# Kernel tuning notes

Measured on AMD Instinct MI355X. Metric: run time of the kernel, lower is better.

The kernel has to match this reference:

```python
import jax, jax.numpy as jnp
import numpy as np

B, K, D = 128, 64, 1536        # batch, image regions, CNN feature dim
EM, H, A = 512, 1024, 1024     # embedding, hidden, attention dims
VOCAB, MAX_LEN = 10000, 30


def setup_inputs() -> dict:
    key = jax.random.key(0)
    ks = jax.random.split(key, 20)
    def p(i, shape):
        return jax.random.normal(ks[i], shape, dtype=jnp.float32) * 0.02
    z = lambda *s: jnp.zeros(s, jnp.float32)
    return {
        "im_input": jax.random.normal(ks[0], (B, K, D), dtype=jnp.float32),
        "w_input": jax.random.randint(ks[1], (B, MAX_LEN + 1), 0, VOCAB),
        "caption_lengths": jax.random.randint(ks[2], (B,), 2, MAX_LEN + 2),
        "emb": p(3, (VOCAB, EM)),
        "W_enc": p(4, (D, H)), "b_enc": z(H),
        "W_glob": p(5, (D, EM)), "b_glob": z(EM),
        "W_ih": p(6, (2 * EM, 4 * H)), "b_ih": z(4 * H),
        "W_hh": p(7, (H, 4 * H)), "b_hh": z(4 * H),
        "W_xg": p(8, (2 * EM, H)), "b_xg": z(H),
        "W_hg": p(9, (H, H)), "b_hg": z(H),
        "Wv": p(10, (H, A)), "bv": z(A),
        "Ws": p(11, (H, A)), "bs": z(A),
        "Wh": p(12, (H, A)), "bh": z(A),
        "wa": p(13, (A, 1)), "ba": z(1),
        "W_out": p(14, (H, VOCAB)), "b_out": z(VOCAB),
    }


def _forward(im_input, emb, W_enc, b_enc, W_glob, b_glob, W_ih, b_ih, W_hh, b_hh,
             W_xg, b_xg, W_hg, b_hg, Wv, bv, Ws, bs, Wh, bh, wa, ba, W_out, b_out,
             w_input, caption_lengths):
    # ImageEncoder: per-region features (B,K,H) and global feature (B,EM)
    V = jax.nn.relu(jnp.einsum('bkd,dh->bkh', im_input, W_enc) + b_enc)
    g = jax.nn.relu(jnp.mean(im_input, axis=1) @ W_glob + b_glob)
    # sort batch by caption length, descending (as in the torch forward)
    order = jnp.argsort(-caption_lengths)
    w = w_input[order]
    g = g[order]
    V = V[order]
    lens = caption_lengths[order] - 1  # has_end_seq_token=True
    target = w[:, 1:]
    h0 = jnp.zeros((B, H), jnp.float32)
    c0 = jnp.zeros((B, H), jnp.float32)

    # Full-batch scan is math-equivalent to the dynamic batch_size_t slicing:
    # lengths are sorted descending, so rows that go inactive never become
    # active again; their masked predictions stay zero, matching the original.
    def step(carry, t):
        h, c = carry
        x = jnp.concatenate([emb[w[:, t]], g], axis=1)  # (B, 2*EM)
        # SentinelLSTM: standard LSTM cell + visual sentinel gate
        gates = x @ W_ih + b_ih + h @ W_hh + b_hh
        i_g, f_g, g_g, o_g = jnp.split(gates, 4, axis=1)
        c_new = jax.nn.sigmoid(f_g) * c + jax.nn.sigmoid(i_g) * jnp.tanh(g_g)
        h_new = jax.nn.sigmoid(o_g) * jnp.tanh(c_new)
        s = jax.nn.sigmoid(x @ W_xg + b_xg + h @ W_hg + b_hg) * jnp.tanh(c_new)
        # Adaptive attention over K regions + sentinel
        hp = h_new @ Wh + bh                                      # (B,A)
        zv = (jnp.tanh(V @ Wv + bv + hp[:, None, :]) @ wa)[..., 0] + ba  # (B,K)
        zs = jnp.tanh(s @ Ws + bs + hp) @ wa + ba                  # (B,1)
        alpha = jax.nn.softmax(jnp.concatenate([zv, zs], axis=1), axis=1)  # (B,K+1)
        ctx = jnp.einsum('bk,bkh->bh', alpha[:, :-1], V)
        beta = alpha[:, -1:]
        z_t = beta * s + (1.0 - beta) * ctx + h_new
        # MultimodalDecoder (decoding_stack_size=1 -> single projection)
        probs = jax.nn.softmax(z_t @ W_out + b_out, axis=1)        # (B,VOCAB)
        probs = jnp.where((t < lens)[:, None], probs, 0.0)
        return (h_new, c_new), probs

    _, P = jax.lax.scan(step, (h0, c0), jnp.arange(MAX_LEN))
    predictions = jnp.transpose(P, (1, 0, 2))  # (B, MAX_LEN, VOCAB)
    return predictions, target, lens


def reference(im_input, w_input, caption_lengths, emb, W_enc, b_enc, W_glob, b_glob,
              W_ih, b_ih, W_hh, b_hh, W_xg, b_xg, W_hg, b_hg, Wv, bv, Ws, bs,
              Wh, bh, wa, ba, W_out, b_out):
    return _forward(im_input, emb, W_enc, b_enc, W_glob, b_glob, W_ih, b_ih,
                    W_hh, b_hh, W_xg, b_xg, W_hg, b_hg, Wv, bv, Ws, bs, Wh, bh,
                    wa, ba, W_out, b_out, w_input, caption_lengths)
```

## Files before the change

### kernel.cpp

```cpp
#include <hip/hip_runtime.h>
#include <math.h>

#define NB 128
#define NKK 64
#define ND 1536
#define NEM 512
#define NH 1024
#define NVOC 10000
#define NT 30
#define CHT 6

#define BM 128
#define BN 64
#define BK 64

typedef __bf16 bf16x8 __attribute__((ext_vector_type(8)));
typedef __bf16 bf16x4 __attribute__((ext_vector_type(4)));
typedef float f32x4 __attribute__((ext_vector_type(4)));

__device__ __forceinline__ float ftanh(float x) {
    float e = __expf(2.f * x);
    return 1.f - 2.f * __builtin_amdgcn_rcpf(e + 1.f);
}
__device__ __forceinline__ float fsig(float x) {
    return __builtin_amdgcn_rcpf(1.f + __expf(-x));
}

__global__ void sort_kernel(const int* __restrict__ cap, const int* __restrict__ w,
                            float* __restrict__ out_target, float* __restrict__ out_lens,
                            int* __restrict__ order, int* __restrict__ lens_s,
                            int* __restrict__ widx) {
    __shared__ int lcap[NB];
    __shared__ int sord[NB];
    int b = threadIdx.x;
    lcap[b] = cap[b];
    __syncthreads();
    int lb = lcap[b];
    int pos = 0;
    for (int j = 0; j < NB; j++) {
        int lj = lcap[j];
        if (lj > lb || (lj == lb && j < b)) pos++;
    }
    sord[pos] = b;
    __syncthreads();
    int src = sord[b];
    order[b] = src;
    int ln = lcap[src] - 1;
    lens_s[b] = ln;
    out_lens[b] = (float)ln;
    for (int j = 0; j < NT; j++)
        out_target[b * NT + j] = (float)w[src * (NT + 1) + j + 1];
    for (int t = 0; t < NT; t++)
        widx[t * NB + b] = w[src * (NT + 1) + t];
}

__global__ void init_kernel(float* __restrict__ c, float* __restrict__ ghh0,
                            float* __restrict__ ghh1) {
    int tid = blockIdx.x * 256 + threadIdx.x;
    if (tid < NB * NH) c[tid] = 0.f;
    if (tid < NB * 5120) { ghh0[tid] = 0.f; ghh1[tid] = 0.f; }
}

__global__ void meanim_kernel(const float* __restrict__ im, const int* __restrict__ order,
                              __bf16* __restrict__ meanb) {
    int b = blockIdx.x;
    int src = order[b];
    const float* base = im + (size_t)src * NKK * ND;
    for (int d = threadIdx.x; d < ND; d += 256) {
        float acc = 0.f;
        for (int k = 0; k < NKK; k++) acc += base[(size_t)k * ND + d];
        meanb[b * ND + d] = (__bf16)(acc * (1.0f / NKK));
    }
}

__global__ void conv_perm_kernel(const float* __restrict__ im, const int* __restrict__ order,
                                 __bf16* __restrict__ imb) {
    int e8 = blockIdx.x * 256 + threadIdx.x;
    size_t elem = (size_t)e8 * 8;
    int bp = (int)(elem / (NKK * ND));
    size_t rem = elem % (NKK * ND);
    const float* src = im + (size_t)order[bp] * NKK * ND + rem;
    float4 f0 = *(const float4*)(src);
    float4 f1 = *(const float4*)(src + 4);
    bf16x8 v = {(__bf16)f0.x, (__bf16)f0.y, (__bf16)f0.z, (__bf16)f0.w,
                (__bf16)f1.x, (__bf16)f1.y, (__bf16)f1.z, (__bf16)f1.w};
    *(bf16x8*)(imb + elem) = v;
}

__global__ __launch_bounds__(256) void transpose_pack(
    const float* __restrict__ src, int ldn, int K, int N,
    __bf16* __restrict__ dst, int ldk) {
    __shared__ float tile[64][65];
    int k0 = blockIdx.y * 64, n0 = blockIdx.x * 64;
    int t = threadIdx.x;
    int kr = t >> 2, nc0 = (t & 3) * 16;
    int kk = k0 + kr;
#pragma unroll
    for (int j = 0; j < 16; j += 4) {
        int nn = n0 + nc0 + j;
        float4 v = make_float4(0.f, 0.f, 0.f, 0.f);
        if (kk < K && nn + 3 < N) v = *(const float4*)(src + (size_t)kk * ldn + nn);
        else if (kk < K) {
            float tmp[4] = {0.f, 0.f, 0.f, 0.f};
            for (int q = 0; q < 4; q++) if (nn + q < N) tmp[q] = src[(size_t)kk * ldn + nn + q];
            v = make_float4(tmp[0], tmp[1], tmp[2], tmp[3]);
        }
        tile[kr][nc0 + j + 0] = v.x; tile[kr][nc0 + j + 1] = v.y;
        tile[kr][nc0 + j + 2] = v.z; tile[kr][nc0 + j + 3] = v.w;
    }
    __syncthreads();
    int nr = t >> 2, kc0 = (t & 3) * 16;
    if (n0 + nr < N) {
        __bf16* drow = dst + (size_t)(n0 + nr) * ldk + k0 + kc0;
#pragma unroll
        for (int j = 0; j < 16; j++)
            if (k0 + kc0 + j < K) drow[j] = (__bf16)tile[kc0 + j][nr];
    }
}

__global__ void conv_bf16_vec(const float* __restrict__ src, __bf16* __restrict__ dst, int n4) {
    int id = blockIdx.x * 256 + threadIdx.x;
    if (id < n4) {
        float4 v = *(const float4*)(src + (size_t)id * 4);
        __bf16* d = dst + (size_t)id * 4;
        d[0] = (__bf16)v.x; d[1] = (__bf16)v.y; d[2] = (__bf16)v.z; d[3] = (__bf16)v.w;
    }
}

__global__ void pack_biases(const float* __restrict__ b_ih, const float* __restrict__ b_hh,
                            const float* __restrict__ b_xg, const float* __restrict__ b_hg,
                            const float* __restrict__ bh, const float* __restrict__ bs,
                            float* __restrict__ bstep, float* __restrict__ b2) {
    int i = blockIdx.x * 256 + threadIdx.x;
    if (i < 4096) bstep[i] = b_ih[i] + b_hh[i];
    else bstep[i] = b_xg[i - 4096] + b_hg[i - 4096];
    if (i < 1024) b2[i] = bh[i];
    else if (i < 2048) b2[i] = bs[i - 1024];
}

template <int AMODE, bool RELU, bool OUTBF>
__global__ __launch_bounds__(256) void gemm_k(
    const void* __restrict__ Aptr, int lda,
    const __bf16* __restrict__ Bt, int ldb,
    const float* __restrict__ bias,
    void* __restrict__ Cptr, int ldc,
    int N, int K,
    const int* __restrict__ widx,
    const __bf16* __restrict__ embb, const __bf16* __restrict__ gbf,
    int swz) {
    const int t = threadIdx.x;
    const int lane = t & 63;
    const int wid = t >> 6;
    const int wr = wid >> 1, wc = wid & 1;
    int bx = blockIdx.x, by = blockIdx.y;
    if (swz) {
        int L = by * gridDim.x + bx;
        int xcd = L & 7, q = L >> 3;
        by = xcd * (gridDim.y >> 3) + q / gridDim.x;
        bx = q % gridDim.x;
    }
    const int m0 = by * BM;
    const int n0 = bx * BN;
    const int lr = lane & 15, lg = lane >> 4, lr8 = lr & 7;

    __shared__ __bf16 As[BM * BK];
    __shared__ __bf16 Bs[BN * BK];

    f32x4 acc[4][2];
#pragma unroll
    for (int i = 0; i < 4; i++)
#pragma unroll
        for (int j = 0; j < 2; j++) acc[i][j] = (f32x4){0.f, 0.f, 0.f, 0.f};

    const int s_row = t >> 1;
    const int s_g0 = (t & 1) * 4;
    const int s_col = t >> 2;
    const int s_bg0 = (t & 3) * 2;
    const int r8 = s_row & 7, c8 = s_col & 7;
    const int aw0 = (s_row << 6) + (((s_g0 + 0) ^ r8) << 3);
    const int aw1 = (s_row << 6) + (((s_g0 + 1) ^ r8) << 3);
    const int aw2 = (s_row << 6) + (((s_g0 + 2) ^ r8) << 3);
    const int aw3 = (s_row << 6) + (((s_g0 + 3) ^ r8) << 3);
    const int bw0 = (s_col << 6) + (((s_bg0 + 0) ^ c8) << 3);
    const int bw1 = (s_col << 6) + (((s_bg0 + 1) ^ c8) << 3);
    const int rA0 = (wr * 64 + 0 * 16 + lr) << 6;
    const int rA1 = (wr * 64 + 1 * 16 + lr) << 6;
    const int rA2 = (wr * 64 + 2 * 16 + lr) << 6;
    const int rA3 = (wr * 64 + 3 * 16 + lr) << 6;
    const int cB0 = (wc * 32 + 0 * 16 + lr) << 6;
    const int cB1 = (wc * 32 + 1 * 16 + lr) << 6;

    const __bf16* a_srcb = nullptr;
    const __bf16* e_base = nullptr;
    const __bf16* g_base = nullptr;
    if (AMODE == 1) {
        int r = m0 + s_row;
        e_base = embb + (size_t)widx[r] * NEM + s_g0 * 8;
        g_base = gbf + (size_t)(r & 127) * NEM + s_g0 * 8 - NEM;
    } else {
        a_srcb = (const __bf16*)Aptr + (size_t)(m0 + s_row) * lda + s_g0 * 8;
    }
    const __bf16* b_src = Bt + (size_t)(n0 + s_col) * ldb + s_bg0 * 8;
    const bool b_ok = (n0 + s_col) < N;

    auto loadA = [&](int k0, bf16x8& a0, bf16x8& a1, bf16x8& a2, bf16x8& a3) {
        if (AMODE == 1) {
            int kk = k0 + s_g0 * 8;
            const bf16x8* p = (const bf16x8*)((kk < NEM ? e_base : g_base) + k0);
            a0 = p[0]; a1 = p[1]; a2 = p[2]; a3 = p[3];
        } else {
            const bf16x8* p = (const bf16x8*)(a_srcb + k0);
            a0 = p[0]; a1 = p[1]; a2 = p[2]; a3 = p[3];
        }
    };
    auto loadB = [&](int k0, bf16x8& b0, bf16x8& b1) {
        if (b_ok) {
            const bf16x8* p = (const bf16x8*)(b_src + k0);
            b0 = p[0]; b1 = p[1];
        } else {
            bf16x8 zv = {};
            b0 = zv; b1 = zv;
        }
    };
    auto writeS = [&](bf16x8 a0, bf16x8 a1, bf16x8 a2, bf16x8 a3, bf16x8 b0, bf16x8 b1) {
        *(bf16x8*)&As[aw0] = a0; *(bf16x8*)&As[aw1] = a1;
        *(bf16x8*)&As[aw2] = a2; *(bf16x8*)&As[aw3] = a3;
        *(bf16x8*)&Bs[bw0] = b0; *(bf16x8*)&Bs[bw1] = b1;
    };
    auto compute = [&]() {
#pragma unroll
        for (int ks = 0; ks < 2; ks++) {
            const int gsw = ((ks * 4 + lg) ^ lr8) << 3;
            bf16x8 af0 = *(const bf16x8*)&As[rA0 + gsw];
            bf16x8 af1 = *(const bf16x8*)&As[rA1 + gsw];
            bf16x8 af2 = *(const bf16x8*)&As[rA2 + gsw];
            bf16x8 af3 = *(const bf16x8*)&As[rA3 + gsw];
            bf16x8 bv0 = *(const bf16x8*)&Bs[cB0 + gsw];
            bf16x8 bv1 = *(const bf16x8*)&Bs[cB1 + gsw];
            acc[0][0] = __builtin_amdgcn_mfma_f32_16x16x32_bf16(af0, bv0, acc[0][0], 0, 0, 0);
            acc[0][1] = __builtin_amdgcn_mfma_f32_16x16x32_bf16(af0, bv1, acc[0][1], 0, 0, 0);
            acc[1][0] = __builtin_amdgcn_mfma_f32_16x16x32_bf16(af1, bv0, acc[1][0], 0, 0, 0);
            acc[1][1] = __builtin_amdgcn_mfma_f32_16x16x32_bf16(af1, bv1, acc[1][1], 0, 0, 0);
            acc[2][0] = __builtin_amdgcn_mfma_f32_16x16x32_bf16(af2, bv0, acc[2][0], 0, 0, 0);
            acc[2][1] = __builtin_amdgcn_mfma_f32_16x16x32_bf16(af2, bv1, acc[2][1], 0, 0, 0);
            acc[3][0] = __builtin_amdgcn_mfma_f32_16x16x32_bf16(af3, bv0, acc[3][0], 0, 0, 0);
            acc[3][1] = __builtin_amdgcn_mfma_f32_16x16x32_bf16(af3, bv1, acc[3][1], 0, 0, 0);
        }
    };

    bf16x8 a0, a1, a2, a3, b0, b1;
    bf16x8 c0, c1, c2, c3, d0, d1;
    loadA(0, a0, a1, a2, a3);
    loadB(0, b0, b1);
    for (int k0 = 0; k0 < K; k0 += 2 * BK) {
        writeS(a0, a1, a2, a3, b0, b1);
        __syncthreads();
        loadA(k0 + BK, c0, c1, c2, c3);
        loadB(k0 + BK, d0, d1);
        compute();
        __syncthreads();
        writeS(c0, c1, c2, c3, d0, d1);
        __syncthreads();
        if (k0 + 2 * BK < K) {
            loadA(k0 + 2 * BK, a0, a1, a2, a3);
            loadB(k0 + 2 * BK, b0, b1);
        }
        compute();
        __syncthreads();
    }

    float* Cf = (float*)Cptr;
    __bf16* Cb = (__bf16*)Cptr;
#pragma unroll
    for (int mi = 0; mi < 4; mi++) {
#pragma unroll
        for (int ni = 0; ni < 2; ni++) {
            int col = n0 + wc * 32 + ni * 16 + lr;
            if (col < N) {
                float bb = bias[col];
#pragma unroll
                for (int rr = 0; rr < 4; rr++) {
                    int row = m0 + wr * 64 + mi * 16 + lg * 4 + rr;
                    float v = acc[mi][ni][rr] + bb;
                    if (RELU) v = fmaxf(v, 0.f);
                    if (OUTBF) Cb[(size_t)row * ldc + col] = (__bf16)v;
                    else Cf[(size_t)row * ldc + col] = v;
                }
            }
        }
    }
}

__device__ __forceinline__ void step_gemm(
    __bf16* As, __bf16* Bs,
    const __bf16* __restrict__ Ab, int lda,
    const __bf16* __restrict__ Bt, int ldb,
    const float* __restrict__ bias,
    float* __restrict__ C, int ldc, int N, int n0, int K) {
    const int t = threadIdx.x;
    const int lane = t & 63;
    const int wid = t >> 6;
    const int wr = wid >> 1, wc = wid & 1;
    const int lr = lane & 15, lg = lane >> 4, lr8 = lr & 7;

    f32x4 acc[4][2];
#pragma unroll
    for (int i = 0; i < 4; i++)
#pragma unroll
        for (int j = 0; j < 2; j++) acc[i][j] = (f32x4){0.f, 0.f, 0.f, 0.f};

    const int s_row = t >> 1;
    const int s_g0 = (t & 1) * 4;
    const int s_col = t >> 2;
    const int s_bg0 = (t & 3) * 2;
    const int r8 = s_row & 7, c8 = s_col & 7;
    const int aw0 = (s_row << 6) + (((s_g0 + 0) ^ r8) << 3);
    const int aw1 = (s_row << 6) + (((s_g0 + 1) ^ r8) << 3);
    const int aw2 = (s_row << 6) + (((s_g0 + 2) ^ r8) << 3);
    const int aw3 = (s_row << 6) + (((s_g0 + 3) ^ r8) << 3);
    const int bw0 = (s_col << 6) + (((s_bg0 + 0) ^ c8) << 3);
    const int bw1 = (s_col << 6) + (((s_bg0 + 1) ^ c8) << 3);
    const int rA0 = (wr * 64 + 0 * 16 + lr) << 6;
    const int rA1 = (wr * 64 + 1 * 16 + lr) << 6;
    const int rA2 = (wr * 64 + 2 * 16 + lr) << 6;
    const int rA3 = (wr * 64 + 3 * 16 + lr) << 6;
    const int cB0 = (wc * 32 + 0 * 16 + lr) << 6;
    const int cB1 = (wc * 32 + 1 * 16 + lr) << 6;

    const __bf16* a_src = Ab + (size_t)s_row * lda + s_g0 * 8;
    const __bf16* b_src = Bt + (size_t)(n0 + s_col) * ldb + s_bg0 * 8;
    const bool b_ok = (n0 + s_col) < N;

    auto loadA = [&](int k0, bf16x8& a0, bf16x8& a1, bf16x8& a2, bf16x8& a3) {
        const bf16x8* p = (const bf16x8*)(a_src + k0);
        a0 = p[0]; a1 = p[1]; a2 = p[2]; a3 = p[3];
    };
    auto loadB = [&](int k0, bf16x8& b0, bf16x8& b1) {
        if (b_ok) {
            const bf16x8* p = (const bf16x8*)(b_src + k0);
            b0 = p[0]; b1 = p[1];
        } else {
            bf16x8 zv = {};
            b0 = zv; b1 = zv;
        }
    };
    auto writeS = [&](bf16x8 a0, bf16x8 a1, bf16x8 a2, bf16x8 a3, bf16x8 b0, bf16x8 b1) {
        *(bf16x8*)&As[aw0] = a0; *(bf16x8*)&As[aw1] = a1;
        *(bf16x8*)&As[aw2] = a2; *(bf16x8*)&As[aw3] = a3;
        *(bf16x8*)&Bs[bw0] = b0; *(bf16x8*)&Bs[bw1] = b1;
    };
    auto compute = [&]() {
#pragma unroll
        for (int ks = 0; ks < 2; ks++) {
            const int gsw = ((ks * 4 + lg) ^ lr8) << 3;
            bf16x8 af0 = *(const bf16x8*)&As[rA0 + gsw];
            bf16x8 af1 = *(const bf16x8*)&As[rA1 + gsw];
            bf16x8 af2 = *(const bf16x8*)&As[rA2 + gsw];
            bf16x8 af3 = *(const bf16x8*)&As[rA3 + gsw];
            bf16x8 bv0 = *(const bf16x8*)&Bs[cB0 + gsw];
            bf16x8 bv1 = *(const bf16x8*)&Bs[cB1 + gsw];
            acc[0][0] = __builtin_amdgcn_mfma_f32_16x16x32_bf16(af0, bv0, acc[0][0], 0, 0, 0);
            acc[0][1] = __builtin_amdgcn_mfma_f32_16x16x32_bf16(af0, bv1, acc[0][1], 0, 0, 0);
            acc[1][0] = __builtin_amdgcn_mfma_f32_16x16x32_bf16(af1, bv0, acc[1][0], 0, 0, 0);
            acc[1][1] = __builtin_amdgcn_mfma_f32_16x16x32_bf16(af1, bv1, acc[1][1], 0, 0, 0);
            acc[2][0] = __builtin_amdgcn_mfma_f32_16x16x32_bf16(af2, bv0, acc[2][0], 0, 0, 0);
            acc[2][1] = __builtin_amdgcn_mfma_f32_16x16x32_bf16(af2, bv1, acc[2][1], 0, 0, 0);
            acc[3][0] = __builtin_amdgcn_mfma_f32_16x16x32_bf16(af3, bv0, acc[3][0], 0, 0, 0);
            acc[3][1] = __builtin_amdgcn_mfma_f32_16x16x32_bf16(af3, bv1, acc[3][1], 0, 0, 0);
        }
    };

    bf16x8 a0, a1, a2, a3, b0, b1;
    bf16x8 c0, c1, c2, c3, d0, d1;
    loadA(0, a0, a1, a2, a3);
    loadB(0, b0, b1);
    for (int k0 = 0; k0 < K; k0 += 2 * BK) {
        writeS(a0, a1, a2, a3, b0, b1);
        __syncthreads();
        loadA(k0 + BK, c0, c1, c2, c3);
        loadB(k0 + BK, d0, d1);
        compute();
        __syncthreads();
        writeS(c0, c1, c2, c3, d0, d1);
        __syncthreads();
        if (k0 + 2 * BK < K) {
            loadA(k0 + 2 * BK, a0, a1, a2, a3);
            loadB(k0 + 2 * BK, b0, b1);
        }
        compute();
        __syncthreads();
    }

#pragma unroll
    for (int mi = 0; mi < 4; mi++) {
#pragma unroll
        for (int ni = 0; ni < 2; ni++) {
            int col = n0 + wc * 32 + ni * 16 + lr;
            if (col < N) {
                float bb = bias ? bias[col] : 0.f;
#pragma unroll
                for (int rr = 0; rr < 4; rr++) {
                    int row = wr * 64 + mi * 16 + lg * 4 + rr;
                    C[(size_t)row * ldc + col] = acc[mi][ni][rr] + bb;
                }
            }
        }
    }
}

__global__ __launch_bounds__(256) void lstm_kernel(
    const __bf16* __restrict__ Xpre, const float* __restrict__ g0,
    const float* __restrict__ g1, float* __restrict__ c,
    __bf16* __restrict__ H_all, __bf16* __restrict__ S_all, int t) {
    int i4 = (blockIdx.x * 256 + threadIdx.x) * 4;
    int b = i4 >> 10, j = i4 & 1023;
    const __bf16* xp = Xpre + ((size_t)t * NB + b) * 5120 + j;
    const float* p0 = g0 + (size_t)b * 5120 + j;
    const float* p1 = g1 + (size_t)b * 5120 + j;
    bf16x4 xi = *(const bf16x4*)(xp);
    bf16x4 xf = *(const bf16x4*)(xp + 1024);
    bf16x4 xg = *(const bf16x4*)(xp + 2048);
    bf16x4 xo = *(const bf16x4*)(xp + 3072);
    bf16x4 xs = *(const bf16x4*)(xp + 4096);
    float4 gi0 = *(const float4*)(p0), gi1 = *(const float4*)(p1);
    float4 gf0 = *(const float4*)(p0 + 1024), gf1 = *(const float4*)(p1 + 1024);
    float4 gg0 = *(const float4*)(p0 + 2048), gg1 = *(const float4*)(p1 + 2048);
    float4 go0 = *(const float4*)(p0 + 3072), go1 = *(const float4*)(p1 + 3072);
    float4 gs0 = *(const float4*)(p0 + 4096), gs1 = *(const float4*)(p1 + 4096);
    float4 cv = *(const float4*)(c + i4);
    float ia[4] = {gi0.x + gi1.x, gi0.y + gi1.y, gi0.z + gi1.z, gi0.w + gi1.w};
    float fa[4] = {gf0.x + gf1.x, gf0.y + gf1.y, gf0.z + gf1.z, gf0.w + gf1.w};
    float ga[4] = {gg0.x + gg1.x, gg0.y + gg1.y, gg0.z + gg1.z, gg0.w + gg1.w};
    float oa[4] = {go0.x + go1.x, go0.y + go1.y, go0.z + go1.z, go0.w + go1.w};
    float sa[4] = {gs0.x + gs1.x, gs0.y + gs1.y, gs0.z + gs1.z, gs0.w + gs1.w};
    float cvp[4] = {cv.x, cv.y, cv.z, cv.w};
    float cn4[4];
    bf16x4 hv, sv;
#pragma unroll
    for (int e = 0; e < 4; e++) {
        float ig = fsig((float)xi[e] + ia[e]);
        float fg = fsig((float)xf[e] + fa[e]);
        float gv = ftanh((float)xg[e] + ga[e]);
        float og = fsig((float)xo[e] + oa[e]);
        float sg = fsig((float)xs[e] + sa[e]);
        float cn = fg * cvp[e] + ig * gv;
        float tc = ftanh(cn);
        cn4[e] = cn;
        hv[e] = (__bf16)(og * tc);
        sv[e] = (__bf16)(sg * tc);
    }
    *(float4*)(c + i4) = make_float4(cn4[0], cn4[1], cn4[2], cn4[3]);
    *(bf16x4*)(H_all + (size_t)t * NB * NH + i4) = hv;
    *(bf16x4*)(S_all + (size_t)t * NB * NH + i4) = sv;
}

__global__ __launch_bounds__(256) void gatesHH_kernel(
    const __bf16* __restrict__ H_t, const __bf16* __restrict__ Whh,
    float* __restrict__ g0, float* __restrict__ g1) {
    __shared__ __bf16 As[BM * BK];
    __shared__ __bf16 Bs[BN * BK];
    int kc = blockIdx.x & 1, n = blockIdx.x >> 1;
    step_gemm(As, Bs, H_t + kc * 512, NH, Whh + kc * 512, 2048, nullptr,
              kc == 0 ? g0 : g1, 5120, 5120, n * 64, 512);
}

__global__ __launch_bounds__(256) void attn_all_kernel(
    const __bf16* __restrict__ VA, const __bf16* __restrict__ V,
    const __bf16* __restrict__ HPa, const __bf16* __restrict__ SWSa,
    const float* __restrict__ wa, const __bf16* __restrict__ H_all,
    const __bf16* __restrict__ S_all, __bf16* __restrict__ Z_all) {
    __shared__ float zscore[NKK + 1];
    __shared__ float alpha_s[NKK + 1];
    int tb = blockIdx.x;
    int b = tb & 127;
    int wave = threadIdx.x >> 6, lane = threadIdx.x & 63;

    float hp_reg[16], wa_reg[16];
    {
        const bf16x8* hr = (const bf16x8*)(HPa + (size_t)tb * NH + lane * 16);
        bf16x8 h0 = hr[0], h1 = hr[1];
        const float* wb = wa + lane * 16;
#pragma unroll
        for (int q = 0; q < 4; q++) {
            float4 wv = *(const float4*)(wb + q * 4);
            wa_reg[q * 4 + 0] = wv.x; wa_reg[q * 4 + 1] = wv.y;
            wa_reg[q * 4 + 2] = wv.z; wa_reg[q * 4 + 3] = wv.w;
        }
#pragma unroll
        for (int j = 0; j < 8; j++) { hp_reg[j] = (float)h0[j]; hp_reg[8 + j] = (float)h1[j]; }
    }
    for (int k = wave; k <= NKK; k += 4) {
        float p = 0.f;
        if (k < NKK) {
            const bf16x8* row = (const bf16x8*)(VA + ((size_t)(b * NKK + k)) * NH + lane * 16);
            bf16x8 v0 = row[0], v1 = row[1];
#pragma unroll
            for (int j = 0; j < 8; j++) {
                p += ftanh((float)v0[j] + hp_reg[j]) * wa_reg[j];
                p += ftanh((float)v1[j] + hp_reg[8 + j]) * wa_reg[8 + j];
            }
        } else {
            const bf16x8* sr = (const bf16x8*)(SWSa + (size_t)tb * NH + lane * 16);
            bf16x8 s0 = sr[0], s1 = sr[1];
#pragma unroll
            for (int j = 0; j < 8; j++) {
                p += ftanh((float)s0[j] + hp_reg[j]) * wa_reg[j];
                p += ftanh((float)s1[j] + hp_reg[8 + j]) * wa_reg[8 + j];
            }
        }
        for (int off = 32; off; off >>= 1) p += __shfl_down(p, off);
        if (lane == 0) zscore[k] = p;
    }
    __syncthreads();
    if (threadIdx.x == 0) {
        float mx = zscore[0];
        for (int i = 1; i <= NKK; i++) mx = fmaxf(mx, zscore[i]);
        float ssum = 0.f;
        for (int i = 0; i <= NKK; i++) { float e = __expf(zscore[i] - mx); alpha_s[i] = e; ssum += e; }
        float inv = __builtin_amdgcn_rcpf(ssum);
        for (int i = 0; i <= NKK; i++) alpha_s[i] *= inv;
    }
    __syncthreads();
    float beta = alpha_s[NKK];
    {
        int jj0 = threadIdx.x * 4;
        const __bf16* vp = V + ((size_t)b * NKK) * NH + jj0;
        float c0 = 0.f, c1 = 0.f, c2 = 0.f, c3 = 0.f;
#pragma unroll 8
        for (int k = 0; k < NKK; k++) {
            bf16x4 vv = *(const bf16x4*)(vp + (size_t)k * NH);
            float a = alpha_s[k];
            c0 += a * (float)vv[0]; c1 += a * (float)vv[1];
            c2 += a * (float)vv[2]; c3 += a * (float)vv[3];
        }
        bf16x4 s4 = *(const bf16x4*)(S_all + (size_t)tb * NH + jj0);
        bf16x4 h4 = *(const bf16x4*)(H_all + (size_t)tb * NH + jj0);
        float ob = 1.f - beta;
        bf16x4 zv;
        zv[0] = (__bf16)(beta * (float)s4[0] + ob * c0 + (float)h4[0]);
        zv[1] = (__bf16)(beta * (float)s4[1] + ob * c1 + (float)h4[1]);
        zv[2] = (__bf16)(beta * (float)s4[2] + ob * c2 + (float)h4[2]);
        zv[3] = (__bf16)(beta * (float)s4[3] + ob * c3 + (float)h4[3]);
        *(bf16x4*)(Z_all + (size_t)tb * NH + jj0) = zv;
    }
}

__global__ __launch_bounds__(256) void softmax_chunk_kernel(
    const float* __restrict__ logitsC, const int* __restrict__ lens,
    float* __restrict__ pred, int t0) {
    __shared__ float se[NVOC];
    __shared__ float sred[4], sred2[4];
    int r = blockIdx.x;
    int tt = r >> 7, b = r & 127;
    int t = t0 + tt;
    float* out = pred + (size_t)b * NT * NVOC + (size_t)t * NVOC;
    if (t >= lens[b]) {
        for (int v = threadIdx.x; v < NVOC; v += 256) out[v] = 0.f;
        return;
    }
    const float* lg = logitsC + (size_t)r * NVOC;
    float mx = -1e30f;
    for (int v = threadIdx.x; v < NVOC; v += 256) {
        float x = lg[v];
        se[v] = x;
        mx = fmaxf(mx, x);
    }
    for (int off = 32; off; off >>= 1) mx = fmaxf(mx, __shfl_down(mx, off));
    if ((threadIdx.x & 63) == 0) sred[threadIdx.x >> 6] = mx;
    __syncthreads();
    mx = fmaxf(fmaxf(sred[0], sred[1]), fmaxf(sred[2], sred[3]));
    float ssum = 0.f;
    for (int v = threadIdx.x; v < NVOC; v += 256) {
        float e = __expf(se[v] - mx);
        se[v] = e;
        ssum += e;
    }
    for (int off = 32; off; off >>= 1) ssum += __shfl_down(ssum, off);
    if ((threadIdx.x & 63) == 0) sred2[threadIdx.x >> 6] = ssum;
    __syncthreads();
    ssum = sred2[0] + sred2[1] + sred2[2] + sred2[3];
    float inv = 1.f / ssum;
    for (int v = threadIdx.x; v < NVOC; v += 256) out[v] = se[v] * inv;
}

extern "C" void kernel_launch(void* const* d_in, const int* in_sizes, int n_in,
                              void* d_out, int out_size, void* d_ws, size_t ws_size,
                              hipStream_t stream) {
    const float* im = (const float*)d_in[0];
    const int* w_in = (const int*)d_in[1];
    const int* cap = (const int*)d_in[2];
    const float* emb = (const float*)d_in[3];
    const float* W_enc = (const float*)d_in[4];
    const float* b_enc = (const float*)d_in[5];
    const float* W_glob = (const float*)d_in[6];
    const float* b_glob = (const float*)d_in[7];
    const float* W_ih = (const float*)d_in[8];
    const float* b_ih = (const float*)d_in[9];
    const float* W_hh = (const float*)d_in[10];
    const float* b_hh = (const float*)d_in[11];
    const float* W_xg = (const float*)d_in[12];
    const float* b_xg = (const float*)d_in[13];
    const float* W_hg = (const float*)d_in[14];
    const float* b_hg = (const float*)d_in[15];
    const float* Wv = (const float*)d_in[16];
    const float* bv = (const float*)d_in[17];
    const float* Ws = (const float*)d_in[18];
    const float* bs = (const float*)d_in[19];
    const float* Wh = (const float*)d_in[20];
    const float* bh = (const float*)d_in[21];
    const float* wa = (const float*)d_in[22];
    const float* W_out = (const float*)d_in[24];
    const float* b_out = (const float*)d_in[25];

    float* out = (float*)d_out;
    float* pred = out;
    float* out_target = out + (size_t)NB * NT * NVOC;
    float* out_lens = out_target + NB * NT;

    char* p = (char*)d_ws;
    size_t off = 0;
    auto carve = [&](size_t bytes) {
        void* r = p + off;
        off += (bytes + 255) & ~(size_t)255;
        return r;
    };
    int* order = (int*)carve(NB * 4);
    int* lens_s = (int*)carve(NB * 4);
    int* widx = (int*)carve(NT * NB * 4);
    __bf16* embb = (__bf16*)carve((size_t)NVOC * NEM * 2);
    __bf16* Wstep_t = (__bf16*)carve((size_t)5120 * 2048 * 2);
    __bf16* W2t = (__bf16*)carve((size_t)2 * 1024 * 1024 * 2);
    __bf16* Wout_t = (__bf16*)carve((size_t)NVOC * 1024 * 2);
    __bf16* Wglob_t = (__bf16*)carve((size_t)512 * 1536 * 2);
    __bf16* Wenc_t = (__bf16*)carve((size_t)1024 * 1536 * 2);
    __bf16* Wv_t = (__bf16*)carve((size_t)1024 * 1024 * 2);
    float* bstep = (float*)carve(5120 * 4);
    float* b2 = (float*)carve(2048 * 4);
    __bf16* meanb = (__bf16*)carve((size_t)NB * ND * 2);
    __bf16* g_bf = (__bf16*)carve((size_t)NB * NEM * 2);
    __bf16* V_bf = (__bf16*)carve((size_t)NB * NKK * NH * 2);
    __bf16* VA_bf = (__bf16*)carve((size_t)NB * NKK * NH * 2);
    void* uni = carve((size_t)NT * NB * 5120 * 2);
    __bf16* imb = (__bf16*)uni;
    __bf16* Xpre = (__bf16*)uni;
    float* logitsC = (float*)uni;
    float* ghh0 = (float*)carve((size_t)NB * 5120 * 4);
    float* ghh1 = (float*)carve((size_t)NB * 5120 * 4);
    float* c = (float*)carve((size_t)NB * NH * 4);
    __bf16* H_all = (__bf16*)carve((size_t)NT * NB * NH * 2);
    __bf16* S_all = (__bf16*)carve((size_t)NT * NB * NH * 2);
    __bf16* HPa = (__bf16*)carve((size_t)NT * NB * NH * 2);
    __bf16* SWSa = (__bf16*)carve((size_t)NT * NB * NH * 2);
    __bf16* Z_all = (__bf16*)carve((size_t)NT * NB * NH * 2);
    if (off > ws_size) return;
    size_t off_save = off;
    float* logitsF = (float*)carve((size_t)NT * NB * NVOC * 4);
    bool useFull = (off <= ws_size);
    if (!useFull) off = off_save;

    sort_kernel<<<1, NB, 0, stream>>>(cap, w_in, out_target, out_lens, order, lens_s, widx);
    init_kernel<<<(NB * 5120 + 255) / 256, 256, 0, stream>>>(c, ghh0, ghh1);
    pack_biases<<<20, 256, 0, stream>>>(b_ih, b_hh, b_xg, b_hg, bh, bs, bstep, b2);
    conv_bf16_vec<<<(NVOC * NEM / 4 + 255) / 256, 256, 0, stream>>>(emb, embb, NVOC * NEM / 4);
    transpose_pack<<<dim3(8, 24), 256, 0, stream>>>(W_glob, 512, 1536, 512, Wglob_t, 1536);
    transpose_pack<<<dim3(16, 24), 256, 0, stream>>>(W_enc, 1024, 1536, 1024, Wenc_t, 1536);
    transpose_pack<<<dim3(16, 16), 256, 0, stream>>>(Wv, 1024, 1024, 1024, Wv_t, 1024);
    transpose_pack<<<dim3(64, 16), 256, 0, stream>>>(W_ih, 4096, 1024, 4096, Wstep_t, 2048);
    transpose_pack<<<dim3(64, 16), 256, 0, stream>>>(W_hh, 4096, 1024, 4096, Wstep_t + 1024, 2048);
    transpose_pack<<<dim3(16, 16), 256, 0, stream>>>(W_xg, 1024, 1024, 1024,
                                                     Wstep_t + (size_t)4096 * 2048, 2048);
    transpose_pack<<<dim3(16, 16), 256, 0, stream>>>(W_hg, 1024, 1024, 1024,
                                                     Wstep_t + (size_t)4096 * 2048 + 1024, 2048);
    transpose_pack<<<dim3(16, 16), 256, 0, stream>>>(Wh, 1024, 1024, 1024, W2t, 1024);
    transpose_pack<<<dim3(16, 16), 256, 0, stream>>>(Ws, 1024, 1024, 1024,
                                                     W2t + (size_t)1024 * 1024, 1024);
    transpose_pack<<<dim3(157, 16), 256, 0, stream>>>(W_out, NVOC, 1024, NVOC, Wout_t, 1024);
    meanim_kernel<<<NB, 256, 0, stream>>>(im, order, meanb);
    conv_perm_kernel<<<(NB * NKK * ND / 8) / 256, 256, 0, stream>>>(im, order, imb);

    gemm_k<0, true, true><<<dim3(NEM / BN, 1), 256, 0, stream>>>(
        meanb, ND, Wglob_t, ND, b_glob, g_bf, NEM, NEM, ND, nullptr, nullptr, nullptr, 0);
    gemm_k<0, true, true><<<dim3(NH / BN, (NB * NKK) / BM), 256, 0, stream>>>(
        imb, ND, Wenc_t, ND, b_enc, V_bf, NH, NH, ND, nullptr, nullptr, nullptr, 1);
    gemm_k<0, false, true><<<dim3(NH / BN, (NB * NKK) / BM), 256, 0, stream>>>(
        V_bf, NH, Wv_t, NH, bv, VA_bf, NH, NH, NH, nullptr, nullptr, nullptr, 1);
    gemm_k<1, false, true><<<dim3(5120 / BN, (NT * NB) / BM), 256, 0, stream>>>(
        nullptr, 0, Wstep_t, 2048, bstep, Xpre, 5120, 5120, 1024, widx, embb, g_bf, 0);

    for (int t = 0; t < NT; t++) {
        lstm_kernel<<<128, 256, 0, stream>>>(Xpre, ghh0, ghh1, c, H_all, S_all, t);
        if (t < NT - 1)
            gatesHH_kernel<<<160, 256, 0, stream>>>(
                H_all + (size_t)t * NB * NH, Wstep_t + 1024, ghh0, ghh1);
    }

    gemm_k<0, false, true><<<dim3(NH / BN, NT), 256, 0, stream>>>(
        H_all, NH, W2t, NH, b2, HPa, NH, NH, NH, nullptr, nullptr, nullptr, 0);
    gemm_k<0, false, true><<<dim3(NH / BN, NT), 256, 0, stream>>>(
        S_all, NH, W2t + (size_t)1024 * 1024, NH, b2 + 1024, SWSa, NH, NH, NH,
        nullptr, nullptr, nullptr, 0);
    attn_all_kernel<<<NT * NB, 256, 0, stream>>>(VA_bf, V_bf, HPa, SWSa, wa, H_all, S_all, Z_all);

    if (useFull) {
        gemm_k<0, false, false><<<dim3((NVOC + BN - 1) / BN, NT), 256, 0, stream>>>(
            Z_all, NH, Wout_t, NH, b_out, logitsF, NVOC, NVOC, NH, nullptr, nullptr, nullptr, 0);
        softmax_chunk_kernel<<<NT * NB, 256, 0, stream>>>(logitsF, lens_s, pred, 0);
    } else {
        for (int c5 = 0; c5 < NT / CHT; c5++) {
            gemm_k<0, false, false><<<dim3((NVOC + BN - 1) / BN, CHT), 256, 0, stream>>>(
                Z_all + (size_t)c5 * CHT * NB * NH, NH, Wout_t, NH, b_out, logitsC, NVOC,
                NVOC, NH, nullptr, nullptr, nullptr, 0);
            softmax_chunk_kernel<<<CHT * NB, 256, 0, stream>>>(logitsC, lens_s, pred, c5 * CHT);
        }
    }
}
```

Baseline: 1.069 ms.

## Fuse recurrent hidden GEMM with LSTM cell and batch attention projections

Each time step's split-K gatesHH GEMM and its separate elementwise LSTM kernel are replaced by one fused_step kernel. Each of its 16 blocks computes all five gate slices for 64 hidden units over the full K and then applies the cell update directly from registers. This removes the fp32 partial-gate buffers, their zero-init, and half of the per-step launches, but leaves only 16 workgroups busy during the serial recurrence. Separately, the two attention projection GEMMs are merged into one launch using blockIdx.z strides. A new XCD-aware block swizzle is used for the input-gate and output-vocabulary GEMMs, with the vocabulary grid padded to 160 columns.

```diff
diff --git a/kernel.cpp b/kernel.cpp
--- a/kernel.cpp
+++ b/kernel.cpp
@@ -54,11 +54,9 @@
         widx[t * NB + b] = w[src * (NT + 1) + t];
 }
 
-__global__ void init_kernel(float* __restrict__ c, float* __restrict__ ghh0,
-                            float* __restrict__ ghh1) {
+__global__ void init_kernel(float* __restrict__ c) {
     int tid = blockIdx.x * 256 + threadIdx.x;
     if (tid < NB * NH) c[tid] = 0.f;
-    if (tid < NB * 5120) { ghh0[tid] = 0.f; ghh1[tid] = 0.f; }
 }
 
 __global__ void meanim_kernel(const float* __restrict__ im, const int* __restrict__ order,
@@ -147,18 +145,25 @@
     int N, int K,
     const int* __restrict__ widx,
     const __bf16* __restrict__ embb, const __bf16* __restrict__ gbf,
-    int swz) {
+    int swz, size_t sA, size_t sB, size_t sBias, size_t sC) {
     const int t = threadIdx.x;
     const int lane = t & 63;
     const int wid = t >> 6;
     const int wr = wid >> 1, wc = wid & 1;
     int bx = blockIdx.x, by = blockIdx.y;
-    if (swz) {
+    if (swz == 1) {
         int L = by * gridDim.x + bx;
         int xcd = L & 7, q = L >> 3;
         by = xcd * (gridDim.y >> 3) + q / gridDim.x;
         bx = q % gridDim.x;
-    }
+    } else if (swz == 2) {
+        int L = by * gridDim.x + bx;
+        int xcd = L & 7, idx = L >> 3;
+        int nby = gridDim.y;
+        bx = xcd + 8 * (idx / nby);
+        by = idx % nby;
+    }
+    const int z = blockIdx.z;
     const int m0 = by * BM;
     const int n0 = bx * BN;
     const int lr = lane & 15, lg = lane >> 4, lr8 = lr & 7;
@@ -198,9 +203,9 @@
         e_base = embb + (size_t)widx[r] * NEM + s_g0 * 8;
         g_base = gbf + (size_t)(r & 127) * NEM + s_g0 * 8 - NEM;
     } else {
-        a_srcb = (const __bf16*)Aptr + (size_t)(m0 + s_row) * lda + s_g0 * 8;
-    }
-    const __bf16* b_src = Bt + (size_t)(n0 + s_col) * ldb + s_bg0 * 8;
+        a_srcb = (const __bf16*)Aptr + z * sA + (size_t)(m0 + s_row) * lda + s_g0 * 8;
+    }
+    const __bf16* b_src = Bt + z * sB + (size_t)(n0 + s_col) * ldb + s_bg0 * 8;
     const bool b_ok = (n0 + s_col) < N;
 
     auto loadA = [&](int k0, bf16x8& a0, bf16x8& a1, bf16x8& a2, bf16x8& a3) {
@@ -269,15 +274,16 @@
         __syncthreads();
     }
 
-    float* Cf = (float*)Cptr;
-    __bf16* Cb = (__bf16*)Cptr;
+    const float* bias_z = bias + z * sBias;
+    float* Cf = (float*)Cptr + z * sC;
+    __bf16* Cb = (__bf16*)Cptr + z * sC;
 #pragma unroll
     for (int mi = 0; mi < 4; mi++) {
 #pragma unroll
         for (int ni = 0; ni < 2; ni++) {
             int col = n0 + wc * 32 + ni * 16 + lr;
             if (col < N) {
-                float bb = bias[col];
+                float bb = bias_z[col];
 #pragma unroll
                 for (int rr = 0; rr < 4; rr++) {
                     int row = m0 + wr * 64 + mi * 16 + lg * 4 + rr;
@@ -291,177 +297,137 @@
     }
 }
 
-__device__ __forceinline__ void step_gemm(
-    __bf16* As, __bf16* Bs,
-    const __bf16* __restrict__ Ab, int lda,
-    const __bf16* __restrict__ Bt, int ldb,
-    const float* __restrict__ bias,
-    float* __restrict__ C, int ldc, int N, int n0, int K) {
-    const int t = threadIdx.x;
-    const int lane = t & 63;
-    const int wid = t >> 6;
+__global__ __launch_bounds__(256, 1) void fused_step(
+    const __bf16* __restrict__ Xpre, const __bf16* __restrict__ Hprev,
+    const __bf16* __restrict__ Wt,
+    float* __restrict__ c, __bf16* __restrict__ Hout, __bf16* __restrict__ Sout,
+    int t) {
+    const int tid = threadIdx.x;
+    const int lane = tid & 63;
+    const int wid = tid >> 6;
     const int wr = wid >> 1, wc = wid & 1;
     const int lr = lane & 15, lg = lane >> 4, lr8 = lr & 7;
-
-    f32x4 acc[4][2];
-#pragma unroll
-    for (int i = 0; i < 4; i++)
-#pragma unroll
-        for (int j = 0; j < 2; j++) acc[i][j] = (f32x4){0.f, 0.f, 0.f, 0.f};
-
-    const int s_row = t >> 1;
-    const int s_g0 = (t & 1) * 4;
-    const int s_col = t >> 2;
-    const int s_bg0 = (t & 3) * 2;
-    const int r8 = s_row & 7, c8 = s_col & 7;
-    const int aw0 = (s_row << 6) + (((s_g0 + 0) ^ r8) << 3);
-    const int aw1 = (s_row << 6) + (((s_g0 + 1) ^ r8) << 3);
-    const int aw2 = (s_row << 6) + (((s_g0 + 2) ^ r8) << 3);
-    const int aw3 = (s_row << 6) + (((s_g0 + 3) ^ r8) << 3);
-    const int bw0 = (s_col << 6) + (((s_bg0 + 0) ^ c8) << 3);
-    const int bw1 = (s_col << 6) + (((s_bg0 + 1) ^ c8) << 3);
-    const int rA0 = (wr * 64 + 0 * 16 + lr) << 6;
-    const int rA1 = (wr * 64 + 1 * 16 + lr) << 6;
-    const int rA2 = (wr * 64 + 2 * 16 + lr) << 6;
-    const int rA3 = (wr * 64 + 3 * 16 + lr) << 6;
-    const int cB0 = (wc * 32 + 0 * 16 + lr) << 6;
-    const int cB1 = (wc * 32 + 1 * 16 + lr) << 6;
-
-    const __bf16* a_src = Ab + (size_t)s_row * lda + s_g0 * 8;
-    const __bf16* b_src = Bt + (size_t)(n0 + s_col) * ldb + s_bg0 * 8;
-    const bool b_ok = (n0 + s_col) < N;
-
-    auto loadA = [&](int k0, bf16x8& a0, bf16x8& a1, bf16x8& a2, bf16x8& a3) {
-        const bf16x8* p = (const bf16x8*)(a_src + k0);
-        a0 = p[0]; a1 = p[1]; a2 = p[2]; a3 = p[3];
-    };
-    auto loadB = [&](int k0, bf16x8& b0, bf16x8& b1) {
-        if (b_ok) {
-            const bf16x8* p = (const bf16x8*)(b_src + k0);
-            b0 = p[0]; b1 = p[1];
-        } else {
-            bf16x8 zv = {};
-            b0 = zv; b1 = zv;
-        }
-    };
-    auto writeS = [&](bf16x8 a0, bf16x8 a1, bf16x8 a2, bf16x8 a3, bf16x8 b0, bf16x8 b1) {
-        *(bf16x8*)&As[aw0] = a0; *(bf16x8*)&As[aw1] = a1;
-        *(bf16x8*)&As[aw2] = a2; *(bf16x8*)&As[aw3] = a3;
-        *(bf16x8*)&Bs[bw0] = b0; *(bf16x8*)&Bs[bw1] = b1;
-    };
-    auto compute = [&]() {
-#pragma unroll
-        for (int ks = 0; ks < 2; ks++) {
-            const int gsw = ((ks * 4 + lg) ^ lr8) << 3;
-            bf16x8 af0 = *(const bf16x8*)&As[rA0 + gsw];
-            bf16x8 af1 = *(const bf16x8*)&As[rA1 + gsw];
-            bf16x8 af2 = *(const bf16x8*)&As[rA2 + gsw];
-            bf16x8 af3 = *(const bf16x8*)&As[rA3 + gsw];
-            bf16x8 bv0 = *(const bf16x8*)&Bs[cB0 + gsw];
-            bf16x8 bv1 = *(const bf16x8*)&Bs[cB1 + gsw];
-            acc[0][0] = __builtin_amdgcn_mfma_f32_16x16x32_bf16(af0, bv0, acc[0][0], 0, 0, 0);
-            acc[0][1] = __builtin_amdgcn_mfma_f32_16x16x32_bf16(af0, bv1, acc[0][1], 0, 0, 0);
-            acc[1][0] = __builtin_amdgcn_mfma_f32_16x16x32_bf16(af1, bv0, acc[1][0], 0, 0, 0);
-            acc[1][1] = __builtin_amdgcn_mfma_f32_16x16x32_bf16(af1, bv1, acc[1][1], 0, 0, 0);
-            acc[2][0] = __builtin_amdgcn_mfma_f32_16x16x32_bf16(af2, bv0, acc[2][0], 0, 0, 0);
-            acc[2][1] = __builtin_amdgcn_mfma_f32_16x16x32_bf16(af2, bv1, acc[2][1], 0, 0, 0);
-            acc[3][0] = __builtin_amdgcn_mfma_f32_16x16x32_bf16(af3, bv0, acc[3][0], 0, 0, 0);
-            acc[3][1] = __builtin_amdgcn_mfma_f32_16x16x32_bf16(af3, bv1, acc[3][1], 0, 0, 0);
-        }
-    };
-
-    bf16x8 a0, a1, a2, a3, b0, b1;
-    bf16x8 c0, c1, c2, c3, d0, d1;
-    loadA(0, a0, a1, a2, a3);
-    loadB(0, b0, b1);
-    for (int k0 = 0; k0 < K; k0 += 2 * BK) {
-        writeS(a0, a1, a2, a3, b0, b1);
-        __syncthreads();
-        loadA(k0 + BK, c0, c1, c2, c3);
-        loadB(k0 + BK, d0, d1);
-        compute();
-        __syncthreads();
-        writeS(c0, c1, c2, c3, d0, d1);
-        __syncthreads();
-        if (k0 + 2 * BK < K) {
-            loadA(k0 + 2 * BK, a0, a1, a2, a3);
-            loadB(k0 + 2 * BK, b0, b1);
-        }
-        compute();
-        __syncthreads();
-    }
-
-#pragma unroll
-    for (int mi = 0; mi < 4; mi++) {
-#pragma unroll
-        for (int ni = 0; ni < 2; ni++) {
-            int col = n0 + wc * 32 + ni * 16 + lr;
-            if (col < N) {
-                float bb = bias ? bias[col] : 0.f;
-#pragma unroll
-                for (int rr = 0; rr < 4; rr++) {
-                    int row = wr * 64 + mi * 16 + lg * 4 + rr;
-                    C[(size_t)row * ldc + col] = acc[mi][ni][rr] + bb;
+    const int j0 = blockIdx.x * 64;
+
+    __shared__ __bf16 As[BM * BK];
+    __shared__ __bf16 Bs[5 * BN * BK];
+
+    f32x4 acc[5][4][2];
+#pragma unroll
+    for (int q = 0; q < 5; q++)
+#pragma unroll
+        for (int i = 0; i < 4; i++)
+#pragma unroll
+            for (int j = 0; j < 2; j++) acc[q][i][j] = (f32x4){0.f, 0.f, 0.f, 0.f};
+
+    if (t > 0) {
+        const int s_row = tid >> 1;
+        const int s_g0 = (tid & 1) * 4;
+        const int s_col = tid >> 2;
+        const int s_bg0 = (tid & 3) * 2;
+        const int r8 = s_row & 7, c8 = s_col & 7;
+        const int aw0 = (s_row << 6) + (((s_g0 + 0) ^ r8) << 3);
+        const int aw1 = (s_row << 6) + (((s_g0 + 1) ^ r8) << 3);
+        const int aw2 = (s_row << 6) + (((s_g0 + 2) ^ r8) << 3);
+        const int aw3 = (s_row << 6) + (((s_g0 + 3) ^ r8) << 3);
+        const int bw0 = (s_col << 6) + (((s_bg0 + 0) ^ c8) << 3);
+        const int bw1 = (s_col << 6) + (((s_bg0 + 1) ^ c8) << 3);
+        const int rA0 = (wr * 64 + 0 * 16 + lr) << 6;
+        const int rA1 = (wr * 64 + 1 * 16 + lr) << 6;
+        const int rA2 = (wr * 64 + 2 * 16 + lr) << 6;
+        const int rA3 = (wr * 64 + 3 * 16 + lr) << 6;
+        const int cB0 = (wc * 32 + 0 * 16 + lr) << 6;
+        const int cB1 = (wc * 32 + 1 * 16 + lr) << 6;
+
+        const __bf16* a_src = Hprev + (size_t)s_row * NH + s_g0 * 8;
+        const __bf16* b_src[5];
+#pragma unroll
+        for (int q = 0; q < 5; q++)
+            b_src[q] = Wt + (size_t)(q * 1024 + j0 + s_col) * 2048 + 1024 + s_bg0 * 8;
+
+        bf16x8 A0[4], A1[4], B0[5][2], B1[5][2];
+        auto loadA = [&](int k0, bf16x8 (&A)[4]) {
+            const bf16x8* p = (const bf16x8*)(a_src + k0);
+            A[0] = p[0]; A[1] = p[1]; A[2] = p[2]; A[3] = p[3];
+        };
+        auto loadBall = [&](int k0, bf16x8 (&B)[5][2]) {
+#pragma unroll
+            for (int q = 0; q < 5; q++) {
+                const bf16x8* p = (const bf16x8*)(b_src[q] + k0);
+                B[q][0] = p[0]; B[q][1] = p[1];
+            }
+        };
+        auto writeS = [&](bf16x8 (&A)[4], bf16x8 (&B)[5][2]) {
+            *(bf16x8*)&As[aw0] = A[0]; *(bf16x8*)&As[aw1] = A[1];
+            *(bf16x8*)&As[aw2] = A[2]; *(bf16x8*)&As[aw3] = A[3];
+#pragma unroll
+            for (int q = 0; q < 5; q++) {
+                *(bf16x8*)&Bs[q * 4096 + bw0] = B[q][0];
+                *(bf16x8*)&Bs[q * 4096 + bw1] = B[q][1];
+            }
+        };
+        auto compute = [&]() {
+#pragma unroll
+            for (int ks = 0; ks < 2; ks++) {
+                const int gsw = ((ks * 4 + lg) ^ lr8) << 3;
+                bf16x8 af0 = *(const bf16x8*)&As[rA0 + gsw];
+                bf16x8 af1 = *(const bf16x8*)&As[rA1 + gsw];
+                bf16x8 af2 = *(const bf16x8*)&As[rA2 + gsw];
+                bf16x8 af3 = *(const bf16x8*)&As[rA3 + gsw];
+#pragma unroll
+                for (int q = 0; q < 5; q++) {
+                    bf16x8 bv0 = *(const bf16x8*)&Bs[q * 4096 + cB0 + gsw];
+                    bf16x8 bv1 = *(const bf16x8*)&Bs[q * 4096 + cB1 + gsw];
+                    acc[q][0][0] = __builtin_amdgcn_mfma_f32_16x16x32_bf16(af0, bv0, acc[q][0][0], 0, 0, 0);
+                    acc[q][0][1] = __builtin_amdgcn_mfma_f32_16x16x32_bf16(af0, bv1, acc[q][0][1], 0, 0, 0);
+                    acc[q][1][0] = __builtin_amdgcn_mfma_f32_16x16x32_bf16(af1, bv0, acc[q][1][0], 0, 0, 0);
+                    acc[q][1][1] = __builtin_amdgcn_mfma_f32_16x16x32_bf16(af1, bv1, acc[q][1][1], 0, 0, 0);
+                    acc[q][2][0] = __builtin_amdgcn_mfma_f32_16x16x32_bf16(af2, bv0, acc[q][2][0], 0, 0, 0);
+                    acc[q][2][1] = __builtin_amdgcn_mfma_f32_16x16x32_bf16(af2, bv1, acc[q][2][1], 0, 0, 0);
+                    acc[q][3][0] = __builtin_amdgcn_mfma_f32_16x16x32_bf16(af3, bv0, acc[q][3][0], 0, 0, 0);
+                    acc[q][3][1] = __builtin_amdgcn_mfma_f32_16x16x32_bf16(af3, bv1, acc[q][3][1], 0, 0, 0);
                 }
             }
-        }
-    }
-}
-
-__global__ __launch_bounds__(256) void lstm_kernel(
-    const __bf16* __restrict__ Xpre, const float* __restrict__ g0,
-    const float* __restrict__ g1, float* __restrict__ c,
-    __bf16* __restrict__ H_all, __bf16* __restrict__ S_all, int t) {
-    int i4 = (blockIdx.x * 256 + threadIdx.x) * 4;
-    int b = i4 >> 10, j = i4 & 1023;
-    const __bf16* xp = Xpre + ((size_t)t * NB + b) * 5120 + j;
-    const float* p0 = g0 + (size_t)b * 5120 + j;
-    const float* p1 = g1 + (size_t)b * 5120 + j;
-    bf16x4 xi = *(const bf16x4*)(xp);
-    bf16x4 xf = *(const bf16x4*)(xp + 1024);
-    bf16x4 xg = *(const bf16x4*)(xp + 2048);
-    bf16x4 xo = *(const bf16x4*)(xp + 3072);
-    bf16x4 xs = *(const bf16x4*)(xp + 4096);
-    float4 gi0 = *(const float4*)(p0), gi1 = *(const float4*)(p1);
-    float4 gf0 = *(const float4*)(p0 + 1024), gf1 = *(const float4*)(p1 + 1024);
-    float4 gg0 = *(const float4*)(p0 + 2048), gg1 = *(const float4*)(p1 + 2048);
-    float4 go0 = *(const float4*)(p0 + 3072), go1 = *(const float4*)(p1 + 3072);
-    float4 gs0 = *(const float4*)(p0 + 4096), gs1 = *(const float4*)(p1 + 4096);
-    float4 cv = *(const float4*)(c + i4);
-    float ia[4] = {gi0.x + gi1.x, gi0.y + gi1.y, gi0.z + gi1.z, gi0.w + gi1.w};
-    float fa[4] = {gf0.x + gf1.x, gf0.y + gf1.y, gf0.z + gf1.z, gf0.w + gf1.w};
-    float ga[4] = {gg0.x + gg1.x, gg0.y + gg1.y, gg0.z + gg1.z, gg0.w + gg1.w};
-    float oa[4] = {go0.x + go1.x, go0.y + go1.y, go0.z + go1.z, go0.w + go1.w};
-    float sa[4] = {gs0.x + gs1.x, gs0.y + gs1.y, gs0.z + gs1.z, gs0.w + gs1.w};
-    float cvp[4] = {cv.x, cv.y, cv.z, cv.w};
-    float cn4[4];
-    bf16x4 hv, sv;
-#pragma unroll
-    for (int e = 0; e < 4; e++) {
-        float ig = fsig((float)xi[e] + ia[e]);
-        float fg = fsig((float)xf[e] + fa[e]);
-        float gv = ftanh((float)xg[e] + ga[e]);
-        float og = fsig((float)xo[e] + oa[e]);
-        float sg = fsig((float)xs[e] + sa[e]);
-        float cn = fg * cvp[e] + ig * gv;
-        float tc = ftanh(cn);
-        cn4[e] = cn;
-        hv[e] = (__bf16)(og * tc);
-        sv[e] = (__bf16)(sg * tc);
-    }
-    *(float4*)(c + i4) = make_float4(cn4[0], cn4[1], cn4[2], cn4[3]);
-    *(bf16x4*)(H_all + (size_t)t * NB * NH + i4) = hv;
-    *(bf16x4*)(S_all + (size_t)t * NB * NH + i4) = sv;
-}
-
-__global__ __launch_bounds__(256) void gatesHH_kernel(
-    const __bf16* __restrict__ H_t, const __bf16* __restrict__ Whh,
-    float* __restrict__ g0, float* __restrict__ g1) {
-    __shared__ __bf16 As[BM * BK];
-    __shared__ __bf16 Bs[BN * BK];
-    int kc = blockIdx.x & 1, n = blockIdx.x >> 1;
-    step_gemm(As, Bs, H_t + kc * 512, NH, Whh + kc * 512, 2048, nullptr,
-              kc == 0 ? g0 : g1, 5120, 5120, n * 64, 512);
+        };
+
+        loadA(0, A0); loadBall(0, B0);
+        for (int k0 = 0; k0 < 1024; k0 += 2 * BK) {
+            writeS(A0, B0);
+            __syncthreads();
+            loadA(k0 + BK, A1); loadBall(k0 + BK, B1);
+            compute();
+            __syncthreads();
+            writeS(A1, B1);
+            __syncthreads();
+            if (k0 + 2 * BK < 1024) { loadA(k0 + 2 * BK, A0); loadBall(k0 + 2 * BK, B0); }
+            compute();
+            __syncthreads();
+        }
+    }
+
+#pragma unroll
+    for (int mi = 0; mi < 4; mi++) {
+#pragma unroll
+        for (int ni = 0; ni < 2; ni++) {
+            int j = j0 + wc * 32 + ni * 16 + lr;
+#pragma unroll
+            for (int rr = 0; rr < 4; rr++) {
+                int b = wr * 64 + mi * 16 + lg * 4 + rr;
+                const __bf16* xr = Xpre + ((size_t)t * NB + b) * 5120 + j;
+                float gi = acc[0][mi][ni][rr] + (float)xr[0];
+                float gf = acc[1][mi][ni][rr] + (float)xr[1024];
+                float gg = acc[2][mi][ni][rr] + (float)xr[2048];
+                float go = acc[3][mi][ni][rr] + (float)xr[3072];
+                float gs = acc[4][mi][ni][rr] + (float)xr[4096];
+                size_t idx = (size_t)b * NH + j;
+                float cn = fsig(gf) * c[idx] + fsig(gi) * ftanh(gg);
+                float tc = ftanh(cn);
+                c[idx] = cn;
+                Hout[idx] = (__bf16)(fsig(go) * tc);
+                Sout[idx] = (__bf16)(fsig(gs) * tc);
+            }
+        }
+    }
 }
 
 __global__ __launch_bounds__(256) void attn_all_kernel(
@@ -644,8 +610,6 @@
     __bf16* imb = (__bf16*)uni;
     __bf16* Xpre = (__bf16*)uni;
     float* logitsC = (float*)uni;
-    float* ghh0 = (float*)carve((size_t)NB * 5120 * 4);
-    float* ghh1 = (float*)carve((size_t)NB * 5120 * 4);
     float* c = (float*)carve((size_t)NB * NH * 4);
     __bf16* H_all = (__bf16*)carve((size_t)NT * NB * NH * 2);
     __bf16* S_all = (__bf16*)carve((size_t)NT * NB * NH * 2);
@@ -659,7 +623,7 @@
     if (!useFull) off = off_save;
 
     sort_kernel<<<1, NB, 0, stream>>>(cap, w_in, out_target, out_lens, order, lens_s, widx);
-    init_kernel<<<(NB * 5120 + 255) / 256, 256, 0, stream>>>(c, ghh0, ghh1);
+    init_kernel<<<512, 256, 0, stream>>>(c);
     pack_biases<<<20, 256, 0, stream>>>(b_ih, b_hh, b_xg, b_hg, bh, bs, bstep, b2);
     conv_bf16_vec<<<(NVOC * NEM / 4 + 255) / 256, 256, 0, stream>>>(emb, embb, NVOC * NEM / 4);
     transpose_pack<<<dim3(8, 24), 256, 0, stream>>>(W_glob, 512, 1536, 512, Wglob_t, 1536);
@@ -679,37 +643,39 @@
     conv_perm_kernel<<<(NB * NKK * ND / 8) / 256, 256, 0, stream>>>(im, order, imb);
 
     gemm_k<0, true, true><<<dim3(NEM / BN, 1), 256, 0, stream>>>(
-        meanb, ND, Wglob_t, ND, b_glob, g_bf, NEM, NEM, ND, nullptr, nullptr, nullptr, 0);
+        meanb, ND, Wglob_t, ND, b_glob, g_bf, NEM, NEM, ND, nullptr, nullptr, nullptr,
+        0, 0, 0, 0, 0);
     gemm_k<0, true, true><<<dim3(NH / BN, (NB * NKK) / BM), 256, 0, stream>>>(
-        imb, ND, Wenc_t, ND, b_enc, V_bf, NH, NH, ND, nullptr, nullptr, nullptr, 1);
+        imb, ND, Wenc_t, ND, b_enc, V_bf, NH, NH, ND, nullptr, nullptr, nullptr,
+        1, 0, 0, 0, 0);
     gemm_k<0, false, true><<<dim3(NH / BN, (NB * NKK) / BM), 256, 0, stream>>>(
-        V_bf, NH, Wv_t, NH, bv, VA_bf, NH, NH, NH, nullptr, nullptr, nullptr, 1);
+        V_bf, NH, Wv_t, NH, bv, VA_bf, NH, NH, NH, nullptr, nullptr, nullptr,
+        1, 0, 0, 0, 0);
     gemm_k<1, false, true><<<dim3(5120 / BN, (NT * NB) / BM), 256, 0, stream>>>(
-        nullptr, 0, Wstep_t, 2048, bstep, Xpre, 5120, 5120, 1024, widx, embb, g_bf, 0);
+        nullptr, 0, Wstep_t, 2048, bstep, Xpre, 5120, 5120, 1024, widx, embb, g_bf,
+        2, 0, 0, 0, 0);
 
     for (int t = 0; t < NT; t++) {
-        lstm_kernel<<<128, 256, 0, stream>>>(Xpre, ghh0, ghh1, c, H_all, S_all, t);
-        if (t < NT - 1)
-            gatesHH_kernel<<<160, 256, 0, stream>>>(
-                H_all + (size_t)t * NB * NH, Wstep_t + 1024, ghh0, ghh1);
-    }
-
-    gemm_k<0, false, true><<<dim3(NH / BN, NT), 256, 0, stream>>>(
-        H_all, NH, W2t, NH, b2, HPa, NH, NH, NH, nullptr, nullptr, nullptr, 0);
-    gemm_k<0, false, true><<<dim3(NH / BN, NT), 256, 0, stream>>>(
-        S_all, NH, W2t + (size_t)1024 * 1024, NH, b2 + 1024, SWSa, NH, NH, NH,
-        nullptr, nullptr, nullptr, 0);
+        fused_step<<<16, 256, 0, stream>>>(
+            Xpre, t ? H_all + (size_t)(t - 1) * NB * NH : nullptr, Wstep_t, c,
+            H_all + (size_t)t * NB * NH, S_all + (size_t)t * NB * NH, t);
+    }
+
+    gemm_k<0, false, true><<<dim3(NH / BN, NT, 2), 256, 0, stream>>>(
+        H_all, NH, W2t, NH, b2, HPa, NH, NH, NH, nullptr, nullptr, nullptr,
+        2, (size_t)NT * NB * NH, (size_t)NH * NH, (size_t)NH, (size_t)NT * NB * NH);
     attn_all_kernel<<<NT * NB, 256, 0, stream>>>(VA_bf, V_bf, HPa, SWSa, wa, H_all, S_all, Z_all);
 
     if (useFull) {
-        gemm_k<0, false, false><<<dim3((NVOC + BN - 1) / BN, NT), 256, 0, stream>>>(
-            Z_all, NH, Wout_t, NH, b_out, logitsF, NVOC, NVOC, NH, nullptr, nullptr, nullptr, 0);
+        gemm_k<0, false, false><<<dim3(160, NT), 256, 0, stream>>>(
+            Z_all, NH, Wout_t, NH, b_out, logitsF, NVOC, NVOC, NH, nullptr, nullptr, nullptr,
+            2, 0, 0, 0, 0);
         softmax_chunk_kernel<<<NT * NB, 256, 0, stream>>>(logitsF, lens_s, pred, 0);
     } else {
         for (int c5 = 0; c5 < NT / CHT; c5++) {
-            gemm_k<0, false, false><<<dim3((NVOC + BN - 1) / BN, CHT), 256, 0, stream>>>(
+            gemm_k<0, false, false><<<dim3(160, CHT), 256, 0, stream>>>(
                 Z_all + (size_t)c5 * CHT * NB * NH, NH, Wout_t, NH, b_out, logitsC, NVOC,
-                NVOC, NH, nullptr, nullptr, nullptr, 0);
+                NVOC, NH, nullptr, nullptr, nullptr, 2, 0, 0, 0, 0);
             softmax_chunk_kernel<<<CHT * NB, 256, 0, stream>>>(logitsC, lens_s, pred, c5 * CHT);
         }
     }
```

Measured after the change: 2.409 ms. 2.25x slower.
